# Performance work log

Measured on AMD Instinct MI355X. Metric: run time of the kernel, lower is better.

## Reference

```python
import jax, jax.numpy as jnp
import numpy as np

D_MODEL = 512
PROJ = 2 * D_MODEL  # 1024
N_STATES = 32
KSIZE = 4
LN_EPS = 1e-3  # keras LayerNormalization default epsilon


def setup_inputs() -> dict:
    key = jax.random.key(0)
    ks = jax.random.split(key, 16)
    B, L = 2, 2048
    s_in = 1.0 / np.sqrt(D_MODEL)
    s_pr = 1.0 / np.sqrt(PROJ)
    x = jax.random.normal(ks[0], (B, L, D_MODEL), dtype=jnp.float32)
    # LayerNorm params
    ln_gamma = jnp.ones((D_MODEL,), jnp.float32)
    ln_beta = jnp.zeros((D_MODEL,), jnp.float32)
    # dense1 / dense2: d_model -> proj
    W1 = jax.random.normal(ks[1], (D_MODEL, PROJ), jnp.float32) * s_in
    b1 = jnp.zeros((PROJ,), jnp.float32)
    W2 = jax.random.normal(ks[2], (D_MODEL, PROJ), jnp.float32) * s_in
    b2 = jnp.zeros((PROJ,), jnp.float32)
    # depthwise causal conv1d: kernel (K, 1, PROJ) in WIO layout, groups=PROJ
    conv_k = jax.random.normal(ks[3], (KSIZE, 1, PROJ), jnp.float32) * 0.5
    conv_b = jnp.zeros((PROJ,), jnp.float32)
    # SSM params
    A_log = jnp.log(jnp.broadcast_to(jnp.arange(1, N_STATES + 1, dtype=jnp.float32), (PROJ, N_STATES)))
    D_skip = jnp.ones((PROJ,), jnp.float32)
    WB = jax.random.normal(ks[4], (PROJ, N_STATES), jnp.float32) * s_pr
    bB = jnp.zeros((N_STATES,), jnp.float32)
    WC = jax.random.normal(ks[5], (PROJ, N_STATES), jnp.float32) * s_pr
    bC = jnp.zeros((N_STATES,), jnp.float32)
    Wd = jax.random.normal(ks[6], (PROJ, PROJ), jnp.float32) * s_pr
    bd = jnp.zeros((PROJ,), jnp.float32)
    # dense3: proj -> d_model
    W3 = jax.random.normal(ks[7], (PROJ, D_MODEL), jnp.float32) * s_pr
    b3 = jnp.zeros((D_MODEL,), jnp.float32)
    return dict(x=x, ln_gamma=ln_gamma, ln_beta=ln_beta, W1=W1, b1=b1, W2=W2, b2=b2,
                conv_k=conv_k, conv_b=conv_b, A_log=A_log, D_skip=D_skip,
                WB=WB, bB=bB, WC=WC, bC=bC, Wd=Wd, bd=bd, W3=W3, b3=b3)


def _layernorm(x, gamma, beta):
    mu = jnp.mean(x, axis=-1, keepdims=True)
    var = jnp.mean(jnp.square(x - mu), axis=-1, keepdims=True)
    return (x - mu) * jax.lax.rsqrt(var + LN_EPS) * gamma + beta


def _causal_dwconv(x, k, b):
    # x: [B,L,C], k: [K,1,C], depthwise causal conv (left-pad K-1)
    y = jax.lax.conv_general_dilated(
        x, k, window_strides=(1,), padding=[(KSIZE - 1, 0)],
        dimension_numbers=('NWC', 'WIO', 'NWC'), feature_group_count=PROJ)
    return y + b


def _selective_scan(u, delta, A, Bm, Cm, D_skip):
    # u, delta: [B,L,D]; A: [D,N]; Bm, Cm: [B,L,N]; D_skip: [D]
    deltaA = jnp.einsum('bld,dn->bldn', delta, A)                 # [B,L,D,N]
    deltaBu = jnp.einsum('bld,bld,bln->bldn', delta, u, Bm)        # [B,L,D,N]
    # shift deltaA left by one along L, zero at the end (pad trick in source)
    shifted = jnp.concatenate([deltaA[:, 1:], jnp.zeros_like(deltaA[:, :1])], axis=1)
    # reversed cumsum along L, then exp
    e = jnp.exp(jnp.flip(jnp.cumsum(jnp.flip(shifted, axis=1), axis=1), axis=1))
    xs = jnp.cumsum(deltaBu * e, axis=1) / (e + 1e-12)
    y = jnp.einsum('bldn,bln->bld', xs, Cm)
    return y + u * D_skip


def reference(x, ln_gamma, ln_beta, W1, b1, W2, b2, conv_k, conv_b,
              A_log, D_skip, WB, bB, WC, bC, Wd, bd, W3, b3):
    h = _layernorm(x, ln_gamma, ln_beta)
    x1 = h @ W1 + b1                      # [B,L,PROJ]
    x1 = _causal_dwconv(x1, conv_k, conv_b)
    x1 = jax.nn.silu(x1)
    A = -jnp.exp(A_log)                    # [PROJ,N]
    Cm = x1 @ WC + bC                      # [B,L,N]
    Bm = x1 @ WB + bB                      # [B,L,N]
    delta = jax.nn.softplus(x1 @ Wd + bd)  # [B,L,PROJ]
    y = _selective_scan(x1, delta, A, Bm, Cm, D_skip)
    x2 = jax.nn.silu(h @ W2 + b2)
    out = (y * x2) @ W3 + b3 + x           # residual; dropout is identity at inference
    return out
```

## Files before the change

kernel.cpp:

```cpp
#include <hip/hip_runtime.h>
#include <stdint.h>

#define L_SEQ 2048
#define BATCH 2
#define DMODEL 512
#define PROJ 1024
#define NST 32
#define NCATU 1088
#define ROWS (BATCH*L_SEQ)
#define THRESH 50.0f

typedef float f32x4 __attribute__((ext_vector_type(4)));
typedef short short8 __attribute__((ext_vector_type(8)));

__device__ inline float bf2f(unsigned short u){ uint32_t x=((uint32_t)u)<<16; float f; __builtin_memcpy(&f,&x,4); return f; }
__device__ inline unsigned short f2bf(float f){ uint32_t x; __builtin_memcpy(&x,&f,4); uint32_t r=x+0x7FFFu+((x>>16)&1u); return (unsigned short)(r>>16); }
__device__ inline float siluf(float x){ return x/(1.f+__expf(-x)); }
__device__ inline float softplusf(float x){ return x>20.f? x : log1pf(__expf(x)); }

#define AS1(p) ((const __attribute__((address_space(1))) void*)(p))
#define AS3(p) ((__attribute__((address_space(3))) void*)(p))

template<int N> __device__ inline void wait_vmcnt(){
  if constexpr (N==0)      asm volatile("s_waitcnt vmcnt(0)" ::: "memory");
  else if constexpr (N==2) asm volatile("s_waitcnt vmcnt(2)" ::: "memory");
  else if constexpr (N==4) asm volatile("s_waitcnt vmcnt(4)" ::: "memory");
  else if constexpr (N==6) asm volatile("s_waitcnt vmcnt(6)" ::: "memory");
  else                     asm volatile("s_waitcnt vmcnt(8)" ::: "memory");
}

__global__ __launch_bounds__(256)
void prep_kernel(const float* __restrict__ W1, const float* __restrict__ b1,
                 const float* __restrict__ W2, const float* __restrict__ b2,
                 const float* __restrict__ Wd, const float* __restrict__ bd,
                 const float* __restrict__ WB, const float* __restrict__ bB,
                 const float* __restrict__ WC, const float* __restrict__ bC,
                 const float* __restrict__ W3,
                 unsigned short* __restrict__ W12t, unsigned short* __restrict__ Wcatt,
                 unsigned short* __restrict__ W3t, float* __restrict__ bias12,
                 float* __restrict__ biascat)
{
  int i = blockIdx.x*256 + threadIdx.x;
  const int nA = 2048*512;
  const int nB = NCATU*1024;
  const int nC = 512*1024;
  if (i < nA) {
    int n = i >> 9, k = i & 511;
    float v = (n < 1024) ? W1[k*1024 + n] : W2[k*1024 + (n-1024)];
    W12t[i] = f2bf(v);
    return;
  }
  i -= nA;
  if (i < nB) {
    int n = i >> 10, k = i & 1023;
    float v;
    if (n < 1024) v = Wd[k*1024 + n];
    else if (n < 1056) v = WB[k*32 + (n-1024)];
    else v = WC[k*32 + (n-1056)];
    Wcatt[i] = f2bf(v);
    return;
  }
  i -= nB;
  if (i < nC) {
    int n = i >> 10, k = i & 1023;
    W3t[i] = f2bf(W3[k*512 + n]);
    return;
  }
  i -= nC;
  if (i < 2048) { bias12[i] = (i < 1024) ? b1[i] : b2[i-1024]; return; }
  i -= 2048;
  if (i < NCATU) {
    biascat[i] = (i < 1024) ? bd[i] : (i < 1056) ? bB[i-1024] : bC[i-1056];
  }
}

__global__ __launch_bounds__(256)
void ln_kernel(const float* __restrict__ x, const float* __restrict__ gamma,
               const float* __restrict__ beta, unsigned short* __restrict__ H)
{
  int row = blockIdx.x*4 + (threadIdx.x >> 6);
  int lane = threadIdx.x & 63;
  const float4* xr = (const float4*)(x + (size_t)row*DMODEL);
  float4 v0 = xr[lane];
  float4 v1 = xr[lane+64];
  float s = v0.x+v0.y+v0.z+v0.w + v1.x+v1.y+v1.z+v1.w;
  float q = v0.x*v0.x+v0.y*v0.y+v0.z*v0.z+v0.w*v0.w
          + v1.x*v1.x+v1.y*v1.y+v1.z*v1.z+v1.w*v1.w;
#pragma unroll
  for (int m=32;m>0;m>>=1){ s += __shfl_xor(s,m); q += __shfl_xor(q,m); }
  float mu = s*(1.f/DMODEL);
  float var = q*(1.f/DMODEL) - mu*mu;
  float rs = rsqrtf(var + 1e-3f);
  int c0 = lane*4, c1 = 256 + lane*4;
  float4 g0 = *(const float4*)&gamma[c0]; float4 g1 = *(const float4*)&gamma[c1];
  float4 t0 = *(const float4*)&beta[c0];  float4 t1 = *(const float4*)&beta[c1];
  ushort4 o0, o1;
  o0.x = f2bf((v0.x-mu)*rs*g0.x + t0.x);
  o0.y = f2bf((v0.y-mu)*rs*g0.y + t0.y);
  o0.z = f2bf((v0.z-mu)*rs*g0.z + t0.z);
  o0.w = f2bf((v0.w-mu)*rs*g0.w + t0.w);
  o1.x = f2bf((v1.x-mu)*rs*g1.x + t1.x);
  o1.y = f2bf((v1.y-mu)*rs*g1.y + t1.y);
  o1.z = f2bf((v1.z-mu)*rs*g1.z + t1.z);
  o1.w = f2bf((v1.w-mu)*rs*g1.w + t1.w);
  *(ushort4*)&H[(size_t)row*DMODEL + c0] = o0;
  *(ushort4*)&H[(size_t)row*DMODEL + c1] = o1;
}

template<int BM, int BN, int MODE>
__global__ __launch_bounds__(256)
void gemm_bt(const unsigned short* __restrict__ A, const unsigned short* __restrict__ Bt,
             void* __restrict__ Cv, const float* __restrict__ bias,
             const float* __restrict__ res, int M, int N, int K)
{
  constexpr int BK = 64;
  constexpr int AM = 2, AN = 2;
  constexpr int ASEGI = BM*BK/8/256;
  constexpr int BSEGI = BN*BK/8/256;
  constexpr int LPT = ASEGI + BSEGI;
  __shared__ unsigned short As[3][BM*BK];
  __shared__ unsigned short Bs[3][BN*BK];
  int tid = threadIdx.x;
  int lane = tid & 63, wid = tid >> 6;
  int wm = wid >> 1, wn = wid & 1;

  int gx = gridDim.x;
  int nwg = gx * gridDim.y;
  int L = blockIdx.y*gx + blockIdx.x;
  int W = (L & 7)*(nwg >> 3) + (L >> 3);
  int bx = W % gx, by = W / gx;
  int m0 = bx*BM, n0 = by*BN;

  f32x4 acc[AM][AN];
#pragma unroll
  for (int i=0;i<AM;i++)
#pragma unroll
    for (int j=0;j<AN;j++)
#pragma unroll
      for (int e=0;e<4;e++) acc[i][j][e] = 0.f;

  const unsigned short* ap[ASEGI];
  const unsigned short* bp[BSEGI];
#pragma unroll
  for (int j=0;j<ASEGI;j++){
    int s = tid + j*256;
    int row = s >> 3, kc = ((s & 7) ^ (row & 7)) * 8;
    ap[j] = A + (size_t)(m0+row)*K + kc;
  }
#pragma unroll
  for (int j=0;j<BSEGI;j++){
    int s = tid + j*256;
    int row = s >> 3, kc = ((s & 7) ^ (row & 7)) * 8;
    bp[j] = Bt + (size_t)(n0+row)*K + kc;
  }

  auto stage = [&](int buf){
#pragma unroll
    for (int j=0;j<ASEGI;j++){
      __builtin_amdgcn_global_load_lds(AS1(ap[j]), AS3(&As[buf][(size_t)(j*256 + wid*64)*8]), 16, 0, 0);
      ap[j] += BK;
    }
#pragma unroll
    for (int j=0;j<BSEGI;j++){
      __builtin_amdgcn_global_load_lds(AS1(bp[j]), AS3(&Bs[buf][(size_t)(j*256 + wid*64)*8]), 16, 0, 0);
      bp[j] += BK;
    }
  };

  stage(0);
  stage(1);
  int T = K/BK;
  int rb = 0, wb = 2;
  int r = lane & 15, kb = lane >> 4;
  for (int t = 0; t < T; ++t) {
    if (t+1 < T) wait_vmcnt<LPT>();
    else         wait_vmcnt<0>();
    __builtin_amdgcn_s_barrier();
    if (t+2 < T) { stage(wb); wb = (wb==2)?0:wb+1; }
#pragma unroll
    for (int ks=0; ks<2; ++ks) {
      short8 af[AM], bfr[AN];
#pragma unroll
      for (int i=0;i<AM;i++){
        int row = wm*32 + i*16 + r;
        int c = (ks*4 + kb) ^ (r & 7);
        af[i] = *(const short8*)&As[rb][(row*8 + c)*8];
      }
#pragma unroll
      for (int j=0;j<AN;j++){
        int row = wn*32 + j*16 + r;
        int c = (ks*4 + kb) ^ (r & 7);
        bfr[j] = *(const short8*)&Bs[rb][(row*8 + c)*8];
      }
#pragma unroll
      for (int i=0;i<AM;i++)
#pragma unroll
        for (int j=0;j<AN;j++)
          acc[i][j] = __builtin_amdgcn_mfma_f32_16x16x32_bf16(af[i], bfr[j], acc[i][j], 0,0,0);
    }
    rb = (rb==2)?0:rb+1;
  }

  int rr = (lane >> 4)*4, cc = lane & 15;
#pragma unroll
  for (int i=0;i<AM;i++)
#pragma unroll
    for (int j=0;j<AN;j++) {
      int col = n0 + wn*32 + j*16 + cc;
      float bcol = (MODE == 4) ? 0.f : bias[col];
#pragma unroll
      for (int e=0;e<4;e++) {
        int row = m0 + wm*32 + i*16 + rr + e;
        float v = acc[i][j][e];
        if constexpr (MODE == 4) {
          v += bias[row];
          if (row < 1024) v = softplusf(v);
          ((float*)Cv)[(size_t)row*N + col] = v;
        } else if constexpr (MODE == 0) {
          ((unsigned short*)Cv)[(size_t)row*N + col] = f2bf(v + bcol);
        } else {
          v += bcol + res[(size_t)row*N + col];
          ((float*)Cv)[(size_t)row*N + col] = v;
        }
      }
    }
}

__global__ __launch_bounds__(256)
void conv_silu_kernel(const unsigned short* __restrict__ P12, const float* __restrict__ ck,
                      const float* __restrict__ cb, unsigned short* __restrict__ ubf,
                      unsigned short* __restrict__ x2bf)
{
  int gid = blockIdx.x*256 + threadIdx.x;
  int c4 = gid & 511;
  int row = gid >> 9;
  int l = row & (L_SEQ-1);
  if (c4 < 256) {
    int c = c4*4;
    float4 bv = *(const float4*)&cb[c];
    float r0=bv.x, r1=bv.y, r2=bv.z, r3=bv.w;
#pragma unroll
    for (int t=0;t<4;t++){
      int lsrc = l - 3 + t;
      if (lsrc >= 0) {
        ushort4 xv = *(const ushort4*)&P12[(size_t)(row-3+t)*2048 + c];
        float4 kv = *(const float4*)&ck[t*PROJ + c];
        r0 = fmaf(bf2f(xv.x),kv.x,r0);
        r1 = fmaf(bf2f(xv.y),kv.y,r1);
        r2 = fmaf(bf2f(xv.z),kv.z,r2);
        r3 = fmaf(bf2f(xv.w),kv.w,r3);
      }
    }
    ushort4 o;
    o.x=f2bf(siluf(r0)); o.y=f2bf(siluf(r1)); o.z=f2bf(siluf(r2)); o.w=f2bf(siluf(r3));
    *(ushort4*)&ubf[(size_t)row*PROJ + c] = o;
  } else {
    int c = (c4-256)*4;
    ushort4 xv = *(const ushort4*)&P12[(size_t)row*2048 + 1024 + c];
    ushort4 o;
    o.x=f2bf(siluf(bf2f(xv.x))); o.y=f2bf(siluf(bf2f(xv.y)));
    o.z=f2bf(siluf(bf2f(xv.z))); o.w=f2bf(siluf(bf2f(xv.w)));
    *(ushort4*)&x2bf[(size_t)row*PROJ + c] = o;
  }
}

__global__ __launch_bounds__(256)
void tsum_kernel(const float* __restrict__ CT, float* __restrict__ suf8,
                 int* __restrict__ l0out)
{
  int G = blockIdx.x;
  int b = G >> 10, d = G & 1023;
  const float* row = CT + (size_t)d*ROWS + b*L_SEQ;
  int t = threadIdx.x;
  float4 v0 = *(const float4*)&row[t*8];
  float4 v1 = *(const float4*)&row[t*8+4];
  float vals[8] = {v0.x,v0.y,v0.z,v0.w,v1.x,v1.y,v1.z,v1.w};
  float part = 0.f;
#pragma unroll
  for (int i=0;i<8;i++) part += vals[i];
  __shared__ float ps[256];
  ps[t] = part; __syncthreads();
  for (int off=1; off<256; off<<=1){
    float v = (t >= off) ? ps[t-off] : 0.f;
    __syncthreads();
    ps[t] += v;
    __syncthreads();
  }
  float T = ps[255];
  float prefx = ps[t] - part;
  suf8[(size_t)G*(L_SEQ/8) + t] = T - prefx;
  float run = prefx; int cnt = 0;
#pragma unroll
  for (int i=0;i<8;i++){
    float suf_l = T - run;
    cnt += (suf_l >= THRESH) ? 1 : 0;
    run += vals[i];
  }
  __shared__ int cs[256];
  cs[t] = cnt; __syncthreads();
  for (int off=128; off>0; off>>=1){ if (t < off) cs[t] += cs[t+off]; __syncthreads(); }
  if (t == 0) {
    int total = cs[0];
    l0out[G] = total > 0 ? total-1 : 0;
  }
}

__global__ __launch_bounds__(256)
void scan_kernel(const float* __restrict__ CT, const float* __restrict__ suf8,
                 const unsigned short* __restrict__ ubf, const float* __restrict__ A_log,
                 const int* __restrict__ l0arr, float* __restrict__ ystate)
{
  int tid = threadIdx.x;
  int n = tid & 31;
  int G = blockIdx.x*8 + (tid >> 5);
  int b = G >> 10, d = G & 1023;
  float np1 = __expf(A_log[d*NST + n]);
  int myl0 = l0arr[G];
  int base = min(myl0, __shfl_xor(myl0, 32)) & ~7;
  const float* dT = CT + (size_t)d*ROWS + b*L_SEQ;
  const float* Br = CT + (size_t)(1024+n)*ROWS + b*L_SEQ;
  const float* Cr = CT + (size_t)(1056+n)*ROWS + b*L_SEQ;
  const float* s8 = suf8 + (size_t)G*(L_SEQ/8);
  const unsigned short* ub = ubf + (size_t)b*L_SEQ*PROJ + d;
  float* yb = ystate + (size_t)b*L_SEQ*PROJ + d;
  float s = 0.f;
  for (int l = base; l < L_SEQ; l += 8) {
    float4 d0 = *(const float4*)&dT[l];
    float4 d1 = *(const float4*)&dT[l+4];
    float4 B0 = *(const float4*)&Br[l];
    float4 B1 = *(const float4*)&Br[l+4];
    float4 C0 = *(const float4*)&Cr[l];
    float4 C1 = *(const float4*)&Cr[l+4];
    float sufv = s8[l >> 3];
    float dl[8] = {d0.x,d0.y,d0.z,d0.w,d1.x,d1.y,d1.z,d1.w};
    float Bv[8] = {B0.x,B0.y,B0.z,B0.w,B1.x,B1.y,B1.z,B1.w};
    float Cv[8] = {C0.x,C0.y,C0.z,C0.w,C1.x,C1.y,C1.z,C1.w};
    float uu[8];
#pragma unroll
    for (int t=0;t<8;t++) uu[t] = bf2f(ub[(size_t)(l+t)*PROJ]);
    float cum = 0.f;
#pragma unroll
    for (int t=0;t<8;t++){
      cum += dl[t];
      float decay = __expf(-dl[t]*np1);
      s = fmaf(decay, s, dl[t]*uu[t]*Bv[t]);
      float gte = 1.f/(1.f + 1e-12f*__expf(np1*(sufv - cum)));
      float contrib = s*gte*Cv[t];
#pragma unroll
      for (int m=16;m>0;m>>=1) contrib += __shfl_xor(contrib, m);
      if (n == 0) yb[(size_t)(l+t)*PROJ] = contrib;
    }
  }
}

__global__ __launch_bounds__(256)
void zmul_kernel(const float* __restrict__ ystate, const unsigned short* __restrict__ ubf,
                 const unsigned short* __restrict__ x2bf, const float* __restrict__ Dskip,
                 const int* __restrict__ l0arr, unsigned short* __restrict__ zbf)
{
  size_t i = ((size_t)blockIdx.x*256 + threadIdx.x)*4;
  int d = (int)(i & (PROJ-1));
  int row = (int)(i >> 10);
  int l = row & (L_SEQ-1);
  int b = row >> 11;
  int4 l0v = *(const int4*)&l0arr[b*PROJ + d];
  float4 ys = *(const float4*)&ystate[i];
  ys.x = (l >= l0v.x) ? ys.x : 0.f;
  ys.y = (l >= l0v.y) ? ys.y : 0.f;
  ys.z = (l >= l0v.z) ? ys.z : 0.f;
  ys.w = (l >= l0v.w) ? ys.w : 0.f;
  ushort4 uu = *(const ushort4*)&ubf[i];
  ushort4 xx = *(const ushort4*)&x2bf[i];
  float4 Dv = *(const float4*)&Dskip[d];
  ushort4 o;
  o.x = f2bf((ys.x + bf2f(uu.x)*Dv.x)*bf2f(xx.x));
  o.y = f2bf((ys.y + bf2f(uu.y)*Dv.y)*bf2f(xx.y));
  o.z = f2bf((ys.z + bf2f(uu.z)*Dv.z)*bf2f(xx.z));
  o.w = f2bf((ys.w + bf2f(uu.w)*Dv.w)*bf2f(xx.w));
  *(ushort4*)&zbf[i] = o;
}

extern "C" void kernel_launch(void* const* d_in, const int* in_sizes, int n_in,
                              void* d_out, int out_size, void* d_ws, size_t ws_size,
                              hipStream_t stream)
{
  const float* x     = (const float*)d_in[0];
  const float* ln_g  = (const float*)d_in[1];
  const float* ln_b  = (const float*)d_in[2];
  const float* W1    = (const float*)d_in[3];
  const float* b1    = (const float*)d_in[4];
  const float* W2    = (const float*)d_in[5];
  const float* b2    = (const float*)d_in[6];
  const float* convk = (const float*)d_in[7];
  const float* convb = (const float*)d_in[8];
  const float* A_log = (const float*)d_in[9];
  const float* Dskip = (const float*)d_in[10];
  const float* WB    = (const float*)d_in[11];
  const float* bB    = (const float*)d_in[12];
  const float* WC    = (const float*)d_in[13];
  const float* bC    = (const float*)d_in[14];
  const float* Wd    = (const float*)d_in[15];
  const float* bd    = (const float*)d_in[16];
  const float* W3    = (const float*)d_in[17];
  const float* b3    = (const float*)d_in[18];

  char* w = (char*)d_ws;
  auto alloc = [&](size_t bytes){ char* p = w; w += (bytes + 255) & ~(size_t)255; return p; };
  unsigned short* Hbf    = (unsigned short*)alloc((size_t)ROWS*DMODEL*2);
  unsigned short* W12t   = (unsigned short*)alloc((size_t)2048*512*2);
  unsigned short* Wcatt  = (unsigned short*)alloc((size_t)NCATU*1024*2);
  unsigned short* W3t    = (unsigned short*)alloc((size_t)512*1024*2);
  float*          bias12 = (float*)alloc(2048*4);
  float*          biascat= (float*)alloc(NCATU*4);
  unsigned short* P12    = (unsigned short*)alloc((size_t)ROWS*2048*2);
  unsigned short* ubf    = (unsigned short*)alloc((size_t)ROWS*PROJ*2);
  unsigned short* x2bf   = (unsigned short*)alloc((size_t)ROWS*PROJ*2);
  float*          CT     = (float*)alloc((size_t)NCATU*ROWS*4);
  float*          suf8   = (float*)alloc((size_t)2048*(L_SEQ/8)*4);
  int*            l0arr  = (int*)alloc(2048*4);
  float*          ystate = (float*)alloc((size_t)ROWS*PROJ*4);
  unsigned short* zbf    = (unsigned short*)alloc((size_t)ROWS*PROJ*2);

  {
    int total = 2048*512 + NCATU*1024 + 512*1024 + 2048 + NCATU;
    prep_kernel<<<(total+255)/256, 256, 0, stream>>>(W1,b1,W2,b2,Wd,bd,WB,bB,WC,bC,W3,
                                                     W12t,Wcatt,W3t,bias12,biascat);
  }
  ln_kernel<<<ROWS/4, 256, 0, stream>>>(x, ln_g, ln_b, Hbf);

  dim3 g1(ROWS/64, 2048/64);
  gemm_bt<64,64,0><<<g1, 256, 0, stream>>>(Hbf, W12t, P12, bias12, nullptr, ROWS, 2048, DMODEL);

  conv_silu_kernel<<<ROWS*512/256, 256, 0, stream>>>(P12, convk, convb, ubf, x2bf);

  dim3 g2(NCATU/64, ROWS/64);
  gemm_bt<64,64,4><<<g2, 256, 0, stream>>>(Wcatt, ubf, CT, biascat, nullptr, NCATU, ROWS, PROJ);

  tsum_kernel<<<2048, 256, 0, stream>>>(CT, suf8, l0arr);

  scan_kernel<<<2048/8, 256, 0, stream>>>(CT, suf8, ubf, A_log, l0arr, ystate);

  zmul_kernel<<<(ROWS*PROJ/4)/256, 256, 0, stream>>>(ystate, ubf, x2bf, Dskip, l0arr, zbf);

  dim3 g3(ROWS/64, DMODEL/64);
  gemm_bt<64,64,3><<<g3, 256, 0, stream>>>(zbf, W3t, (float*)d_out, b3, x, ROWS, DMODEL, PROJ);
}
```

Before: 160.2 us.

## Fuse suffix-sum into scan, enlarge GEMM tiles, store scan output as bf16

Merges the separate suffix-sum/threshold kernel into the scan kernel, which now computes per-channel totals with warp shuffles and keeps the per-8 suffix values in shared memory, dropping a launch and a global round trip. All three GEMMs move to 128x64 tiles, with the concatenated weight padded from 1088 to 1152 rows so it divides evenly. The scan output is stored as bf16 to halve traffic into the elementwise multiply. Risks include lower occupancy from the larger tiles, extra padded GEMM work, bf16 rounding of the scan output, and redundant re-reads of the delta row by each group of 32 threads.

```diff
diff --git a/kernel.cpp b/kernel.cpp
--- a/kernel.cpp
+++ b/kernel.cpp
@@ -6,7 +6,7 @@
 #define DMODEL 512
 #define PROJ 1024
 #define NST 32
-#define NCATU 1088
+#define NCAT 1152
 #define ROWS (BATCH*L_SEQ)
 #define THRESH 50.0f
 
@@ -23,7 +23,6 @@
 
 template<int N> __device__ inline void wait_vmcnt(){
   if constexpr (N==0)      asm volatile("s_waitcnt vmcnt(0)" ::: "memory");
-  else if constexpr (N==2) asm volatile("s_waitcnt vmcnt(2)" ::: "memory");
   else if constexpr (N==4) asm volatile("s_waitcnt vmcnt(4)" ::: "memory");
   else if constexpr (N==6) asm volatile("s_waitcnt vmcnt(6)" ::: "memory");
   else                     asm volatile("s_waitcnt vmcnt(8)" ::: "memory");
@@ -42,7 +41,7 @@
 {
   int i = blockIdx.x*256 + threadIdx.x;
   const int nA = 2048*512;
-  const int nB = NCATU*1024;
+  const int nB = NCAT*1024;
   const int nC = 512*1024;
   if (i < nA) {
     int n = i >> 9, k = i & 511;
@@ -56,7 +55,8 @@
     float v;
     if (n < 1024) v = Wd[k*1024 + n];
     else if (n < 1056) v = WB[k*32 + (n-1024)];
-    else v = WC[k*32 + (n-1056)];
+    else if (n < 1088) v = WC[k*32 + (n-1056)];
+    else v = 0.f;
     Wcatt[i] = f2bf(v);
     return;
   }
@@ -69,8 +69,8 @@
   i -= nC;
   if (i < 2048) { bias12[i] = (i < 1024) ? b1[i] : b2[i-1024]; return; }
   i -= 2048;
-  if (i < NCATU) {
-    biascat[i] = (i < 1024) ? bd[i] : (i < 1056) ? bB[i-1024] : bC[i-1056];
+  if (i < NCAT) {
+    biascat[i] = (i < 1024) ? bd[i] : (i < 1056) ? bB[i-1024] : (i < 1088) ? bC[i-1056] : 0.f;
   }
 }
 
@@ -114,9 +114,10 @@
              const float* __restrict__ res, int M, int N, int K)
 {
   constexpr int BK = 64;
-  constexpr int AM = 2, AN = 2;
-  constexpr int ASEGI = BM*BK/8/256;
-  constexpr int BSEGI = BN*BK/8/256;
+  constexpr int BMW = BM/2, BNW = BN/2;
+  constexpr int AM = BMW/16, AN = BNW/16;
+  constexpr int ASEGI = BM/32;
+  constexpr int BSEGI = BN/32;
   constexpr int LPT = ASEGI + BSEGI;
   __shared__ unsigned short As[3][BM*BK];
   __shared__ unsigned short Bs[3][BN*BK];
@@ -179,18 +180,17 @@
     if (t+2 < T) { stage(wb); wb = (wb==2)?0:wb+1; }
 #pragma unroll
     for (int ks=0; ks<2; ++ks) {
+      int cx = (ks*4 + kb) ^ (r & 7);
       short8 af[AM], bfr[AN];
 #pragma unroll
       for (int i=0;i<AM;i++){
-        int row = wm*32 + i*16 + r;
-        int c = (ks*4 + kb) ^ (r & 7);
-        af[i] = *(const short8*)&As[rb][(row*8 + c)*8];
+        int row = wm*BMW + i*16 + r;
+        af[i] = *(const short8*)&As[rb][(row*8 + cx)*8];
       }
 #pragma unroll
       for (int j=0;j<AN;j++){
-        int row = wn*32 + j*16 + r;
-        int c = (ks*4 + kb) ^ (r & 7);
-        bfr[j] = *(const short8*)&Bs[rb][(row*8 + c)*8];
+        int row = wn*BNW + j*16 + r;
+        bfr[j] = *(const short8*)&Bs[rb][(row*8 + cx)*8];
       }
 #pragma unroll
       for (int i=0;i<AM;i++)
@@ -206,17 +206,17 @@
   for (int i=0;i<AM;i++)
 #pragma unroll
     for (int j=0;j<AN;j++) {
-      int col = n0 + wn*32 + j*16 + cc;
-      float bcol = (MODE == 4) ? 0.f : bias[col];
+      int col = n0 + wn*BNW + j*16 + cc;
+      float bcol = (MODE == 2) ? 0.f : bias[col];
 #pragma unroll
       for (int e=0;e<4;e++) {
-        int row = m0 + wm*32 + i*16 + rr + e;
+        int row = m0 + wm*BMW + i*16 + rr + e;
         float v = acc[i][j][e];
-        if constexpr (MODE == 4) {
+        if constexpr (MODE == 2) {
           v += bias[row];
           if (row < 1024) v = softplusf(v);
           ((float*)Cv)[(size_t)row*N + col] = v;
-        } else if constexpr (MODE == 0) {
+        } else if constexpr (MODE == 1) {
           ((unsigned short*)Cv)[(size_t)row*N + col] = f2bf(v + bcol);
         } else {
           v += bcol + res[(size_t)row*N + col];
@@ -265,64 +265,52 @@
 }
 
 __global__ __launch_bounds__(256)
-void tsum_kernel(const float* __restrict__ CT, float* __restrict__ suf8,
-                 int* __restrict__ l0out)
-{
-  int G = blockIdx.x;
+void sscan_kernel(const float* __restrict__ CT, const unsigned short* __restrict__ ubf,
+                  const float* __restrict__ A_log, int* __restrict__ l0out,
+                  unsigned short* __restrict__ ystate)
+{
+  __shared__ float suf8sh[8][256];
+  int tid = threadIdx.x;
+  int n = tid & 31, gsub = tid >> 5;
+  int G = blockIdx.x*8 + gsub;
   int b = G >> 10, d = G & 1023;
-  const float* row = CT + (size_t)d*ROWS + b*L_SEQ;
-  int t = threadIdx.x;
-  float4 v0 = *(const float4*)&row[t*8];
-  float4 v1 = *(const float4*)&row[t*8+4];
-  float vals[8] = {v0.x,v0.y,v0.z,v0.w,v1.x,v1.y,v1.z,v1.w};
-  float part = 0.f;
-#pragma unroll
-  for (int i=0;i<8;i++) part += vals[i];
-  __shared__ float ps[256];
-  ps[t] = part; __syncthreads();
-  for (int off=1; off<256; off<<=1){
-    float v = (t >= off) ? ps[t-off] : 0.f;
-    __syncthreads();
-    ps[t] += v;
-    __syncthreads();
-  }
-  float T = ps[255];
-  float prefx = ps[t] - part;
-  suf8[(size_t)G*(L_SEQ/8) + t] = T - prefx;
-  float run = prefx; int cnt = 0;
-#pragma unroll
-  for (int i=0;i<8;i++){
-    float suf_l = T - run;
-    cnt += (suf_l >= THRESH) ? 1 : 0;
-    run += vals[i];
-  }
-  __shared__ int cs[256];
-  cs[t] = cnt; __syncthreads();
-  for (int off=128; off>0; off>>=1){ if (t < off) cs[t] += cs[t+off]; __syncthreads(); }
-  if (t == 0) {
-    int total = cs[0];
-    l0out[G] = total > 0 ? total-1 : 0;
-  }
-}
-
-__global__ __launch_bounds__(256)
-void scan_kernel(const float* __restrict__ CT, const float* __restrict__ suf8,
-                 const unsigned short* __restrict__ ubf, const float* __restrict__ A_log,
-                 const int* __restrict__ l0arr, float* __restrict__ ystate)
-{
-  int tid = threadIdx.x;
-  int n = tid & 31;
-  int G = blockIdx.x*8 + (tid >> 5);
-  int b = G >> 10, d = G & 1023;
+  const float* dT = CT + (size_t)d*ROWS + b*L_SEQ;
+
+  float mysum = 0.f;
+  {
+    const float4* c4 = (const float4*)(dT + n*64);
+    for (int it=0; it<16; ++it){ float4 v = c4[it]; mysum += v.x+v.y+v.z+v.w; }
+  }
+  float incl = mysum;
+#pragma unroll
+  for (int dlt=1; dlt<32; dlt<<=1){ float t = __shfl_up(incl, dlt, 32); if (n >= dlt) incl += t; }
+  float Tot = __shfl(incl, 31, 32);
+  float excl = incl - mysum;
+  int cnt = 0;
+  {
+    const float4* c4 = (const float4*)(dT + n*64);
+    float run = excl;
+    for (int it=0; it<16; ++it){
+      float4 v = c4[it];
+      if ((it & 1) == 0) suf8sh[gsub][n*8 + (it>>1)] = Tot - run;
+      cnt += (Tot - run >= THRESH); run += v.x;
+      cnt += (Tot - run >= THRESH); run += v.y;
+      cnt += (Tot - run >= THRESH); run += v.z;
+      cnt += (Tot - run >= THRESH); run += v.w;
+    }
+  }
+#pragma unroll
+  for (int m=16;m>0;m>>=1) cnt += __shfl_xor(cnt, m, 32);
+  int myl0 = cnt > 0 ? cnt-1 : 0;
+  if (n == 0) l0out[G] = myl0;
+  __syncthreads();
+
+  int base = min(myl0, __shfl_xor(myl0, 32)) & ~7;
   float np1 = __expf(A_log[d*NST + n]);
-  int myl0 = l0arr[G];
-  int base = min(myl0, __shfl_xor(myl0, 32)) & ~7;
-  const float* dT = CT + (size_t)d*ROWS + b*L_SEQ;
   const float* Br = CT + (size_t)(1024+n)*ROWS + b*L_SEQ;
   const float* Cr = CT + (size_t)(1056+n)*ROWS + b*L_SEQ;
-  const float* s8 = suf8 + (size_t)G*(L_SEQ/8);
   const unsigned short* ub = ubf + (size_t)b*L_SEQ*PROJ + d;
-  float* yb = ystate + (size_t)b*L_SEQ*PROJ + d;
+  unsigned short* yb = ystate + (size_t)b*L_SEQ*PROJ + d;
   float s = 0.f;
   for (int l = base; l < L_SEQ; l += 8) {
     float4 d0 = *(const float4*)&dT[l];
@@ -331,7 +319,7 @@
     float4 B1 = *(const float4*)&Br[l+4];
     float4 C0 = *(const float4*)&Cr[l];
     float4 C1 = *(const float4*)&Cr[l+4];
-    float sufv = s8[l >> 3];
+    float sufv = suf8sh[gsub][l >> 3];
     float dl[8] = {d0.x,d0.y,d0.z,d0.w,d1.x,d1.y,d1.z,d1.w};
     float Bv[8] = {B0.x,B0.y,B0.z,B0.w,B1.x,B1.y,B1.z,B1.w};
     float Cv[8] = {C0.x,C0.y,C0.z,C0.w,C1.x,C1.y,C1.z,C1.w};
@@ -348,13 +336,13 @@
       float contrib = s*gte*Cv[t];
 #pragma unroll
       for (int m=16;m>0;m>>=1) contrib += __shfl_xor(contrib, m);
-      if (n == 0) yb[(size_t)(l+t)*PROJ] = contrib;
-    }
-  }
-}
-
-__global__ __launch_bounds__(256)
-void zmul_kernel(const float* __restrict__ ystate, const unsigned short* __restrict__ ubf,
+      if (n == 0) yb[(size_t)(l+t)*PROJ] = f2bf(contrib);
+    }
+  }
+}
+
+__global__ __launch_bounds__(256)
+void zmul_kernel(const unsigned short* __restrict__ ystate, const unsigned short* __restrict__ ubf,
                  const unsigned short* __restrict__ x2bf, const float* __restrict__ Dskip,
                  const int* __restrict__ l0arr, unsigned short* __restrict__ zbf)
 {
@@ -364,19 +352,19 @@
   int l = row & (L_SEQ-1);
   int b = row >> 11;
   int4 l0v = *(const int4*)&l0arr[b*PROJ + d];
-  float4 ys = *(const float4*)&ystate[i];
-  ys.x = (l >= l0v.x) ? ys.x : 0.f;
-  ys.y = (l >= l0v.y) ? ys.y : 0.f;
-  ys.z = (l >= l0v.z) ? ys.z : 0.f;
-  ys.w = (l >= l0v.w) ? ys.w : 0.f;
+  ushort4 yu = *(const ushort4*)&ystate[i];
+  float ysx = (l >= l0v.x) ? bf2f(yu.x) : 0.f;
+  float ysy = (l >= l0v.y) ? bf2f(yu.y) : 0.f;
+  float ysz = (l >= l0v.z) ? bf2f(yu.z) : 0.f;
+  float ysw = (l >= l0v.w) ? bf2f(yu.w) : 0.f;
   ushort4 uu = *(const ushort4*)&ubf[i];
   ushort4 xx = *(const ushort4*)&x2bf[i];
   float4 Dv = *(const float4*)&Dskip[d];
   ushort4 o;
-  o.x = f2bf((ys.x + bf2f(uu.x)*Dv.x)*bf2f(xx.x));
-  o.y = f2bf((ys.y + bf2f(uu.y)*Dv.y)*bf2f(xx.y));
-  o.z = f2bf((ys.z + bf2f(uu.z)*Dv.z)*bf2f(xx.z));
-  o.w = f2bf((ys.w + bf2f(uu.w)*Dv.w)*bf2f(xx.w));
+  o.x = f2bf((ysx + bf2f(uu.x)*Dv.x)*bf2f(xx.x));
+  o.y = f2bf((ysy + bf2f(uu.y)*Dv.y)*bf2f(xx.y));
+  o.z = f2bf((ysz + bf2f(uu.z)*Dv.z)*bf2f(xx.z));
+  o.w = f2bf((ysw + bf2f(uu.w)*Dv.w)*bf2f(xx.w));
   *(ushort4*)&zbf[i] = o;
 }
 
@@ -408,40 +396,37 @@
   auto alloc = [&](size_t bytes){ char* p = w; w += (bytes + 255) & ~(size_t)255; return p; };
   unsigned short* Hbf    = (unsigned short*)alloc((size_t)ROWS*DMODEL*2);
   unsigned short* W12t   = (unsigned short*)alloc((size_t)2048*512*2);
-  unsigned short* Wcatt  = (unsigned short*)alloc((size_t)NCATU*1024*2);
+  unsigned short* Wcatt  = (unsigned short*)alloc((size_t)NCAT*1024*2);
   unsigned short* W3t    = (unsigned short*)alloc((size_t)512*1024*2);
   float*          bias12 = (float*)alloc(2048*4);
-  float*          biascat= (float*)alloc(NCATU*4);
+  float*          biascat= (float*)alloc(NCAT*4);
   unsigned short* P12    = (unsigned short*)alloc((size_t)ROWS*2048*2);
   unsigned short* ubf    = (unsigned short*)alloc((size_t)ROWS*PROJ*2);
   unsigned short* x2bf   = (unsigned short*)alloc((size_t)ROWS*PROJ*2);
-  float*          CT     = (float*)alloc((size_t)NCATU*ROWS*4);
-  float*          suf8   = (float*)alloc((size_t)2048*(L_SEQ/8)*4);
+  float*          CT     = (float*)alloc((size_t)NCAT*ROWS*4);
   int*            l0arr  = (int*)alloc(2048*4);
-  float*          ystate = (float*)alloc((size_t)ROWS*PROJ*4);
+  unsigned short* ystate = (unsigned short*)alloc((size_t)ROWS*PROJ*2);
   unsigned short* zbf    = (unsigned short*)alloc((size_t)ROWS*PROJ*2);
 
   {
-    int total = 2048*512 + NCATU*1024 + 512*1024 + 2048 + NCATU;
+    int total = 2048*512 + NCAT*1024 + 512*1024 + 2048 + NCAT;
     prep_kernel<<<(total+255)/256, 256, 0, stream>>>(W1,b1,W2,b2,Wd,bd,WB,bB,WC,bC,W3,
                                                      W12t,Wcatt,W3t,bias12,biascat);
   }
   ln_kernel<<<ROWS/4, 256, 0, stream>>>(x, ln_g, ln_b, Hbf);
 
-  dim3 g1(ROWS/64, 2048/64);
-  gemm_bt<64,64,0><<<g1, 256, 0, stream>>>(Hbf, W12t, P12, bias12, nullptr, ROWS, 2048, DMODEL);
+  dim3 g1(ROWS/128, 2048/64);
+  gemm_bt<128,64,1><<<g1, 256, 0, stream>>>(Hbf, W12t, P12, bias12, nullptr, ROWS, 2048, DMODEL);
 
   conv_silu_kernel<<<ROWS*512/256, 256, 0, stream>>>(P12, convk, convb, ubf, x2bf);
 
-  dim3 g2(NCATU/64, ROWS/64);
-  gemm_bt<64,64,4><<<g2, 256, 0, stream>>>(Wcatt, ubf, CT, biascat, nullptr, NCATU, ROWS, PROJ);
-
-  tsum_kernel<<<2048, 256, 0, stream>>>(CT, suf8, l0arr);
-
-  scan_kernel<<<2048/8, 256, 0, stream>>>(CT, suf8, ubf, A_log, l0arr, ystate);
+  dim3 g2(NCAT/128, ROWS/64);
+  gemm_bt<128,64,2><<<g2, 256, 0, stream>>>(Wcatt, ubf, CT, biascat, nullptr, NCAT, ROWS, PROJ);
+
+  sscan_kernel<<<2048/8, 256, 0, stream>>>(CT, ubf, A_log, l0arr, ystate);
 
   zmul_kernel<<<(ROWS*PROJ/4)/256, 256, 0, stream>>>(ystate, ubf, x2bf, Dskip, l0arr, zbf);
 
-  dim3 g3(ROWS/64, DMODEL/64);
-  gemm_bt<64,64,3><<<g3, 256, 0, stream>>>(zbf, W3t, (float*)d_out, b3, x, ROWS, DMODEL, PROJ);
-}
+  dim3 g3(ROWS/128, DMODEL/64);
+  gemm_bt<128,64,3><<<g3, 256, 0, stream>>>(zbf, W3t, (float*)d_out, b3, x, ROWS, DMODEL, PROJ);
+}
```

Result: slower. 166.3 us (+3.8%).
